# Optimization experiments

Measured on AMD Instinct MI355X. Metric: run time of the kernel, lower is better.

## Reference

```python
import jax, jax.numpy as jnp
import numpy as np

B, T, D = 2, 2048, 2048
H, KVH, HD = 32, 8, 64
N_REP = H // KVH


def setup_inputs() -> dict:
    key = jax.random.key(0)
    ks = jax.random.split(key, 7)
    x = jax.random.normal(ks[0], (B, T, D), dtype=jnp.float32)
    # rope tables: [max_seq, head_dim//2]
    cos = jax.random.uniform(ks[1], (T, HD // 2), dtype=jnp.float32, minval=-1.0, maxval=1.0)
    sin = jax.random.uniform(ks[2], (T, HD // 2), dtype=jnp.float32, minval=-1.0, maxval=1.0)
    s = 0.02
    wq = jax.random.normal(ks[3], (D, H * HD), dtype=jnp.float32) * s
    wk = jax.random.normal(ks[4], (D, KVH * HD), dtype=jnp.float32) * s
    wv = jax.random.normal(ks[5], (D, KVH * HD), dtype=jnp.float32) * s
    wo = jax.random.normal(ks[6], (H * HD, D), dtype=jnp.float32) * s
    return {"x": x, "cos": cos, "sin": sin, "wq": wq, "wk": wk, "wv": wv, "wo": wo}


def _rotate(t):
    h = t.shape[-1] // 2
    return jnp.concatenate([-t[..., h:], t[..., :h]], axis=-1)


def reference(x, cos, sin, wq, wk, wv, wo):
    b, t, _ = x.shape
    # projections -> [B, heads, T, HD]
    q = (x @ wq).reshape(b, t, H, HD).transpose(0, 2, 1, 3)
    k = (x @ wk).reshape(b, t, KVH, HD).transpose(0, 2, 1, 3)
    v = (x @ wv).reshape(b, t, KVH, HD).transpose(0, 2, 1, 3)
    # rope: cos/sin tiled (concat) to full head_dim, broadcast over batch/head
    cos_f = jnp.tile(cos[:t], (1, 2))[None, None]  # [1,1,T,HD]
    sin_f = jnp.tile(sin[:t], (1, 2))[None, None]
    q = q * cos_f + _rotate(q) * sin_f
    k = k * cos_f + _rotate(k) * sin_f
    # GQA: repeat kv heads
    k = jnp.repeat(k, N_REP, axis=1)
    v = jnp.repeat(v, N_REP, axis=1)
    scale = 1.0 / np.sqrt(HD).astype(np.float32)
    scores = jnp.einsum('bhqd,bhkd->bhqk', q, k) * scale
    causal = jnp.tril(jnp.ones((t, t), dtype=bool))
    scores = jnp.where(causal, scores, jnp.float32(-1e30))
    attn = jax.nn.softmax(scores, axis=-1)
    out = jnp.einsum('bhqk,bhkd->bhqd', attn, v)
    out = out.transpose(0, 2, 1, 3).reshape(b, t, H * HD)
    return out @ wo
```

## Files before the change

### kernel.cpp

```cpp
#include <hip/hip_runtime.h>
#include <hip/hip_bf16.h>
#include <cstdint>

typedef unsigned short u16;
typedef unsigned int u32;
typedef __bf16 bf16x8 __attribute__((ext_vector_type(8)));
typedef float f32x4 __attribute__((ext_vector_type(4)));

#define BATCH 2
#define SEQ 2048
#define DMODEL 2048
#define NH 32
#define NKVH 8
#define HD 64
#define NQROWS (BATCH*SEQ)
#define QCOLS (NH*HD)
#define KVCOLS (NKVH*HD)
#define NCAT (QCOLS+2*KVCOLS)

static __device__ __forceinline__ u16 f2bf(float f) {
  u32 u = __float_as_uint(f);
  return (u16)((u + 0x7fffu + ((u >> 16) & 1u)) >> 16);
}

#define GLOAD16(gp, lp) __builtin_amdgcn_global_load_lds( \
    (const __attribute__((address_space(1))) void*)(gp),  \
    (__attribute__((address_space(3))) void*)(lp), 16, 0, 0)

__global__ __launch_bounds__(256) void k_cvt_bf16(const float* __restrict__ in,
                                                  u16* __restrict__ out, int n4) {
  int i = blockIdx.x * 256 + threadIdx.x;
  if (i >= n4) return;
  float4 v = reinterpret_cast<const float4*>(in)[i];
  ushort4 o;
  o.x = f2bf(v.x); o.y = f2bf(v.y); o.z = f2bf(v.z); o.w = f2bf(v.w);
  reinterpret_cast<ushort4*>(out)[i] = o;
}

__global__ __launch_bounds__(256) void k_transpose_w(const float* __restrict__ in,
                                                     u16* __restrict__ out, int R, int C) {
  __shared__ float tile[32][33];
  int c0 = blockIdx.x * 32, r0 = blockIdx.y * 32;
  int tx = threadIdx.x, ty = threadIdx.y;
#pragma unroll
  for (int i = 0; i < 4; i++)
    tile[ty * 4 + i][tx] = in[(size_t)(r0 + ty * 4 + i) * C + c0 + tx];
  __syncthreads();
#pragma unroll
  for (int i = 0; i < 4; i++)
    out[(size_t)(c0 + ty * 4 + i) * R + r0 + tx] = f2bf(tile[tx][ty * 4 + i]);
}

template<int EPI>
__global__ __launch_bounds__(256) void k_gemm(const u16* __restrict__ A,
                                              const u16* __restrict__ BT,
                                              void* __restrict__ Cout,
                                              int M, int N, int K,
                                              const float* __restrict__ cosb,
                                              const float* __restrict__ sinb,
                                              u16* __restrict__ dstK,
                                              u16* __restrict__ dstV) {
  __shared__ __align__(16) u16 As[128 * 32];
  __shared__ __align__(16) u16 Bs[128 * 32];
  const int tid = threadIdx.x;
  const int w = tid >> 6, l = tid & 63;
  const int l15 = l & 15, l4 = l >> 4;
  const int m0 = blockIdx.y * 128, n0 = blockIdx.x * 128;
  const int wr = w >> 1, wc = w & 1;

  const u16* ga = A + (size_t)(m0 + w * 32 + (l >> 2)) * K + (l & 3) * 8;
  const u16* gb = BT + (size_t)(n0 + w * 32 + (l >> 2)) * K + (l & 3) * 8;
  u16* asb = &As[w * 1024];
  u16* bsb = &Bs[w * 1024];
  const int af_off = (wr * 64 + l15) * 32 + l4 * 8;
  const int bf_off = (wc * 64 + l15) * 32 + l4 * 8;

  f32x4 acc[4][4] = {};
  for (int kt = 0; kt < K; kt += 32) {
    GLOAD16(ga, asb);
    GLOAD16(ga + 16 * (size_t)K, asb + 512);
    GLOAD16(gb, bsb);
    GLOAD16(gb + 16 * (size_t)K, bsb + 512);
    ga += 32; gb += 32;
    __syncthreads();
    bf16x8 af[4], bfv[4];
#pragma unroll
    for (int mi = 0; mi < 4; mi++)
      af[mi] = *reinterpret_cast<const bf16x8*>(&As[af_off + mi * 512]);
#pragma unroll
    for (int ni = 0; ni < 4; ni++)
      bfv[ni] = *reinterpret_cast<const bf16x8*>(&Bs[bf_off + ni * 512]);
#pragma unroll
    for (int mi = 0; mi < 4; mi++)
#pragma unroll
      for (int ni = 0; ni < 4; ni++)
        acc[mi][ni] = __builtin_amdgcn_mfma_f32_16x16x32_bf16(af[mi], bfv[ni], acc[mi][ni], 0, 0, 0);
    __syncthreads();
  }

  const int row0 = m0 + wr * 64 + l4 * 4;
  const int col0 = n0 + wc * 64 + l15;
  if constexpr (EPI == 1) {
    float* C = (float*)Cout;
#pragma unroll
    for (int mi = 0; mi < 4; mi++)
#pragma unroll
      for (int ni = 0; ni < 4; ni++)
#pragma unroll
        for (int j = 0; j < 4; j++)
          C[(size_t)(row0 + mi * 16 + j) * N + col0 + ni * 16] = acc[mi][ni][j];
  } else {
    if (n0 < QCOLS + KVCOLS) {
#pragma unroll
      for (int mi = 0; mi < 4; mi++)
#pragma unroll
        for (int j = 0; j < 4; j++) {
          int t = (row0 + mi * 16 + j) & (SEQ - 1);
#pragma unroll
          for (int ni = 0; ni < 2; ni++) {
            int d = ni * 16 + l15;
            float c = cosb[t * 32 + d], s = sinb[t * 32 + d];
            float a = acc[mi][ni][j], bb = acc[mi][ni + 2][j];
            acc[mi][ni][j]     = a * c - bb * s;
            acc[mi][ni + 2][j] = bb * c + a * s;
          }
        }
      if (n0 < QCOLS) {
        u16* C = (u16*)Cout;
#pragma unroll
        for (int mi = 0; mi < 4; mi++)
#pragma unroll
          for (int ni = 0; ni < 4; ni++)
#pragma unroll
            for (int j = 0; j < 4; j++)
              C[(size_t)(row0 + mi * 16 + j) * QCOLS + col0 + ni * 16] = f2bf(acc[mi][ni][j]);
      } else {
        int kc0 = col0 - QCOLS;
#pragma unroll
        for (int mi = 0; mi < 4; mi++)
#pragma unroll
          for (int ni = 0; ni < 4; ni++)
#pragma unroll
            for (int j = 0; j < 4; j++)
              dstK[(size_t)(row0 + mi * 16 + j) * KVCOLS + kc0 + ni * 16] = f2bf(acc[mi][ni][j]);
      }
    } else {
      int vc0 = col0 - (QCOLS + KVCOLS);
#pragma unroll
      for (int mi = 0; mi < 4; mi++) {
        int row = row0 + mi * 16;
        int b = row >> 11, t = row & (SEQ - 1);
#pragma unroll
        for (int ni = 0; ni < 4; ni++) {
          ushort4 v;
          v.x = f2bf(acc[mi][ni][0]);
          v.y = f2bf(acc[mi][ni][1]);
          v.z = f2bf(acc[mi][ni][2]);
          v.w = f2bf(acc[mi][ni][3]);
          *reinterpret_cast<ushort4*>(&dstV[((size_t)b * KVCOLS + vc0 + ni * 16) * SEQ + t]) = v;
        }
      }
    }
  }
}

__global__ __launch_bounds__(256) void k_attn(const u16* __restrict__ Q,
                                              const u16* __restrict__ K,
                                              const u16* __restrict__ VT,
                                              u16* __restrict__ AO) {
  __shared__ __align__(16) u16 Ks[2][4096];
  __shared__ __align__(16) u16 Vs[2][4096];
  __shared__ __align__(16) u16 Plds[4][32][72];
  const int tid = threadIdx.x;
  const int w = tid >> 6, l = tid & 63;
  const int l15 = l & 15, l4 = l >> 4;
  const int bh = blockIdx.y;
  const int b = bh >> 5, h = bh & 31, g = h >> 2;
  const float cS = 0.125f * 1.44269504088896f;
  const int srow_w = w * 8 + (l >> 3);
  const int sslot = l & 7;

  const u16* Kbase = K + ((size_t)b * SEQ) * KVCOLS + g * 64;
  const u16* Vbase = VT + ((size_t)(b * KVCOLS + g * 64)) * SEQ;

  for (int half = 0; half < 2; half++) {
    const int qt = half ? (15 - blockIdx.x) : blockIdx.x;
    const int qrow0 = qt * 128 + w * 32;
    const int nkc = 2 * qt + 2;

    bf16x8 aQ[2][2];
#pragma unroll
    for (int mf = 0; mf < 2; mf++) {
      const u16* qp = Q + (size_t)(b * SEQ + qrow0 + mf * 16 + l15) * QCOLS + h * 64 + l4 * 8;
      aQ[mf][0] = *reinterpret_cast<const bf16x8*>(qp);
      aQ[mf][1] = *reinterpret_cast<const bf16x8*>(qp + 32);
    }
    f32x4 oacc[2][4] = {};
    float lsumP[2][4] = {};

#pragma unroll
    for (int i = 0; i < 2; i++) {
      int r = i * 32 + srow_w;
      int cs = sslot ^ (r & 7);
      GLOAD16(Kbase + (size_t)r * KVCOLS + cs * 8, &Ks[0][i * 2048 + w * 512 + l * 8]);
      GLOAD16(Vbase + (size_t)r * SEQ + cs * 8, &Vs[0][i * 2048 + w * 512 + l * 8]);
    }
    __syncthreads();

    for (int kc = 0; kc < nkc; kc++) {
      const int bi = kc & 1;
      if (kc + 1 < nkc) {
#pragma unroll
        for (int i = 0; i < 2; i++) {
          int r = i * 32 + srow_w;
          int cs = sslot ^ (r & 7);
          GLOAD16(Kbase + (size_t)((kc + 1) * 64 + r) * KVCOLS + cs * 8,
                  &Ks[bi ^ 1][i * 2048 + w * 512 + l * 8]);
          GLOAD16(Vbase + (size_t)r * SEQ + (kc + 1) * 64 + cs * 8,
                  &Vs[bi ^ 1][i * 2048 + w * 512 + l * 8]);
        }
      }
      const bool skip = (kc * 64 > qrow0 + 31);
      if (!skip) {
        f32x4 sacc[2][4] = {};
#pragma unroll
        for (int ni = 0; ni < 4; ni++) {
          int kr = ni * 16 + l15;
#pragma unroll
          for (int hh = 0; hh < 2; hh++) {
            int slot = (hh * 4 + l4) ^ (kr & 7);
            bf16x8 kf = *reinterpret_cast<const bf16x8*>(&Ks[bi][kr * 64 + slot * 8]);
            sacc[0][ni] = __builtin_amdgcn_mfma_f32_16x16x32_bf16(aQ[0][hh], kf, sacc[0][ni], 0, 0, 0);
            sacc[1][ni] = __builtin_amdgcn_mfma_f32_16x16x32_bf16(aQ[1][hh], kf, sacc[1][ni], 0, 0, 0);
          }
        }
        const bool diag = (kc * 64 + 63 > qrow0);
#pragma unroll
        for (int mf = 0; mf < 2; mf++) {
          int qr = qrow0 + mf * 16 + l4 * 4;
#pragma unroll
          for (int ni = 0; ni < 4; ni++) {
            int kcol = kc * 64 + ni * 16 + l15;
#pragma unroll
            for (int j = 0; j < 4; j++) {
              float pv = exp2f(sacc[mf][ni][j] * cS);
              if (diag && (kcol > qr + j)) pv = 0.f;
              lsumP[mf][j] += pv;
              __bf16 pb = (__bf16)pv;
              Plds[w][mf * 16 + l4 * 4 + j][ni * 16 + l15] = *(u16*)&pb;
            }
          }
        }
#pragma unroll
        for (int mf = 0; mf < 2; mf++) {
          bf16x8 pa0 = *reinterpret_cast<const bf16x8*>(&Plds[w][mf * 16 + l15][l4 * 8]);
          bf16x8 pa1 = *reinterpret_cast<const bf16x8*>(&Plds[w][mf * 16 + l15][32 + l4 * 8]);
#pragma unroll
          for (int no = 0; no < 4; no++) {
            int vr = no * 16 + l15;
            int s0 = l4 ^ (vr & 7);
            int s1 = (4 + l4) ^ (vr & 7);
            bf16x8 v0 = *reinterpret_cast<const bf16x8*>(&Vs[bi][vr * 64 + s0 * 8]);
            bf16x8 v1 = *reinterpret_cast<const bf16x8*>(&Vs[bi][vr * 64 + s1 * 8]);
            oacc[mf][no] = __builtin_amdgcn_mfma_f32_16x16x32_bf16(pa0, v0, oacc[mf][no], 0, 0, 0);
            oacc[mf][no] = __builtin_amdgcn_mfma_f32_16x16x32_bf16(pa1, v1, oacc[mf][no], 0, 0, 0);
          }
        }
      }
      __syncthreads();
    }
#pragma unroll
    for (int mf = 0; mf < 2; mf++) {
#pragma unroll
      for (int j = 0; j < 4; j++) {
        float v = lsumP[mf][j];
        v += __shfl_xor(v, 1, 16);
        v += __shfl_xor(v, 2, 16);
        v += __shfl_xor(v, 4, 16);
        v += __shfl_xor(v, 8, 16);
        float rv = 1.f / v;
        int row = b * SEQ + qrow0 + mf * 16 + l4 * 4 + j;
#pragma unroll
        for (int no = 0; no < 4; no++)
          AO[(size_t)row * QCOLS + h * 64 + no * 16 + l15] = f2bf(oacc[mf][no][j] * rv);
      }
    }
  }
}

extern "C" void kernel_launch(void* const* d_in, const int* in_sizes, int n_in,
                              void* d_out, int out_size, void* d_ws, size_t ws_size,
                              hipStream_t stream) {
  const float* x    = (const float*)d_in[0];
  const float* cosb = (const float*)d_in[1];
  const float* sinb = (const float*)d_in[2];
  const float* wq   = (const float*)d_in[3];
  const float* wk   = (const float*)d_in[4];
  const float* wv   = (const float*)d_in[5];
  const float* wo   = (const float*)d_in[6];
  float* out = (float*)d_out;

  char* ws = (char*)d_ws;
  size_t off = 0;
  auto alloc = [&](size_t bytes) -> void* {
    void* p = ws + off;
    off += (bytes + 255) & ~(size_t)255;
    return p;
  };
  u16* xb    = (u16*)alloc((size_t)NQROWS * DMODEL * 2);
  u16* wcatT = (u16*)alloc((size_t)NCAT * DMODEL * 2);
  u16* woT   = (u16*)alloc((size_t)DMODEL * QCOLS * 2);
  u16* Qb    = (u16*)alloc((size_t)NQROWS * QCOLS * 2);
  u16* Kb    = (u16*)alloc((size_t)NQROWS * KVCOLS * 2);
  u16* VTb   = (u16*)alloc((size_t)BATCH * KVCOLS * SEQ * 2);
  u16* AO    = (u16*)alloc((size_t)NQROWS * QCOLS * 2);

  k_cvt_bf16<<<dim3(NQROWS * DMODEL / 4 / 256), dim3(256), 0, stream>>>(x, xb, NQROWS * DMODEL / 4);
  k_transpose_w<<<dim3(QCOLS / 32, DMODEL / 32), dim3(32, 8), 0, stream>>>(wq, wcatT, DMODEL, QCOLS);
  k_transpose_w<<<dim3(KVCOLS / 32, DMODEL / 32), dim3(32, 8), 0, stream>>>(wk, wcatT + (size_t)QCOLS * DMODEL, DMODEL, KVCOLS);
  k_transpose_w<<<dim3(KVCOLS / 32, DMODEL / 32), dim3(32, 8), 0, stream>>>(wv, wcatT + (size_t)(QCOLS + KVCOLS) * DMODEL, DMODEL, KVCOLS);
  k_transpose_w<<<dim3(DMODEL / 32, QCOLS / 32), dim3(32, 8), 0, stream>>>(wo, woT, QCOLS, DMODEL);

  k_gemm<3><<<dim3(NCAT / 128, NQROWS / 128), 256, 0, stream>>>(
      xb, wcatT, Qb, NQROWS, NCAT, DMODEL, cosb, sinb, Kb, VTb);

  k_attn<<<dim3(8, BATCH * NH), 256, 0, stream>>>(Qb, Kb, VTb, AO);

  k_gemm<1><<<dim3(DMODEL / 128, NQROWS / 128), 256, 0, stream>>>(
      AO, woT, out, NQROWS, DMODEL, QCOLS, nullptr, nullptr, nullptr, nullptr);
}
```

Baseline: 249.3 us.

## Shrink attention query tile to 64 rows per block and double the grid

The attention kernel now gives each block 64 query rows (16 per wave) instead of 128 (32 per wave), and launches twice as many blocks. The paired tiles are folded as qt and 31-qt so per-block causal work stays balanced. Each block now walks fewer K/V chunks, and the per-wave skip check goes away because every chunk up to the diagonal is useful. This adds parallelism and occupancy, lowers register use, and cuts work wasted on masked chunks. In exchange, K/V tiles are reused across only half as many query rows, so K/V global traffic per query doubles.

```diff
diff --git a/kernel.cpp b/kernel.cpp
--- a/kernel.cpp
+++ b/kernel.cpp
@@ -170,7 +170,7 @@
                                               u16* __restrict__ AO) {
   __shared__ __align__(16) u16 Ks[2][4096];
   __shared__ __align__(16) u16 Vs[2][4096];
-  __shared__ __align__(16) u16 Plds[4][32][72];
+  __shared__ __align__(16) u16 Plds[4][16][72];
   const int tid = threadIdx.x;
   const int w = tid >> 6, l = tid & 63;
   const int l15 = l & 15, l4 = l >> 4;
@@ -184,19 +184,18 @@
   const u16* Vbase = VT + ((size_t)(b * KVCOLS + g * 64)) * SEQ;
 
   for (int half = 0; half < 2; half++) {
-    const int qt = half ? (15 - blockIdx.x) : blockIdx.x;
-    const int qrow0 = qt * 128 + w * 32;
-    const int nkc = 2 * qt + 2;
-
-    bf16x8 aQ[2][2];
-#pragma unroll
-    for (int mf = 0; mf < 2; mf++) {
-      const u16* qp = Q + (size_t)(b * SEQ + qrow0 + mf * 16 + l15) * QCOLS + h * 64 + l4 * 8;
-      aQ[mf][0] = *reinterpret_cast<const bf16x8*>(qp);
-      aQ[mf][1] = *reinterpret_cast<const bf16x8*>(qp + 32);
-    }
-    f32x4 oacc[2][4] = {};
-    float lsumP[2][4] = {};
+    const int qt = half ? (31 - blockIdx.x) : blockIdx.x;
+    const int qrow0 = qt * 64 + w * 16;
+    const int nkc = qt + 1;
+
+    bf16x8 aQ[2];
+    {
+      const u16* qp = Q + (size_t)(b * SEQ + qrow0 + l15) * QCOLS + h * 64 + l4 * 8;
+      aQ[0] = *reinterpret_cast<const bf16x8*>(qp);
+      aQ[1] = *reinterpret_cast<const bf16x8*>(qp + 32);
+    }
+    f32x4 oacc[4] = {};
+    float lsumP[4] = {};
 
 #pragma unroll
     for (int i = 0; i < 2; i++) {
@@ -220,70 +219,61 @@
                   &Vs[bi ^ 1][i * 2048 + w * 512 + l * 8]);
         }
       }
-      const bool skip = (kc * 64 > qrow0 + 31);
-      if (!skip) {
-        f32x4 sacc[2][4] = {};
+      f32x4 sacc[4] = {};
+#pragma unroll
+      for (int ni = 0; ni < 4; ni++) {
+        int kr = ni * 16 + l15;
+#pragma unroll
+        for (int hh = 0; hh < 2; hh++) {
+          int slot = (hh * 4 + l4) ^ (kr & 7);
+          bf16x8 kf = *reinterpret_cast<const bf16x8*>(&Ks[bi][kr * 64 + slot * 8]);
+          sacc[ni] = __builtin_amdgcn_mfma_f32_16x16x32_bf16(aQ[hh], kf, sacc[ni], 0, 0, 0);
+        }
+      }
+      const bool diag = (kc == qt);
+      {
+        int qr = qrow0 + l4 * 4;
 #pragma unroll
         for (int ni = 0; ni < 4; ni++) {
-          int kr = ni * 16 + l15;
-#pragma unroll
-          for (int hh = 0; hh < 2; hh++) {
-            int slot = (hh * 4 + l4) ^ (kr & 7);
-            bf16x8 kf = *reinterpret_cast<const bf16x8*>(&Ks[bi][kr * 64 + slot * 8]);
-            sacc[0][ni] = __builtin_amdgcn_mfma_f32_16x16x32_bf16(aQ[0][hh], kf, sacc[0][ni], 0, 0, 0);
-            sacc[1][ni] = __builtin_amdgcn_mfma_f32_16x16x32_bf16(aQ[1][hh], kf, sacc[1][ni], 0, 0, 0);
+          int kcol = kc * 64 + ni * 16 + l15;
+#pragma unroll
+          for (int j = 0; j < 4; j++) {
+            float pv = exp2f(sacc[ni][j] * cS);
+            if (diag && (kcol > qr + j)) pv = 0.f;
+            lsumP[j] += pv;
+            __bf16 pb = (__bf16)pv;
+            Plds[w][l4 * 4 + j][ni * 16 + l15] = *(u16*)&pb;
           }
         }
-        const bool diag = (kc * 64 + 63 > qrow0);
-#pragma unroll
-        for (int mf = 0; mf < 2; mf++) {
-          int qr = qrow0 + mf * 16 + l4 * 4;
-#pragma unroll
-          for (int ni = 0; ni < 4; ni++) {
-            int kcol = kc * 64 + ni * 16 + l15;
-#pragma unroll
-            for (int j = 0; j < 4; j++) {
-              float pv = exp2f(sacc[mf][ni][j] * cS);
-              if (diag && (kcol > qr + j)) pv = 0.f;
-              lsumP[mf][j] += pv;
-              __bf16 pb = (__bf16)pv;
-              Plds[w][mf * 16 + l4 * 4 + j][ni * 16 + l15] = *(u16*)&pb;
-            }
-          }
-        }
-#pragma unroll
-        for (int mf = 0; mf < 2; mf++) {
-          bf16x8 pa0 = *reinterpret_cast<const bf16x8*>(&Plds[w][mf * 16 + l15][l4 * 8]);
-          bf16x8 pa1 = *reinterpret_cast<const bf16x8*>(&Plds[w][mf * 16 + l15][32 + l4 * 8]);
-#pragma unroll
-          for (int no = 0; no < 4; no++) {
-            int vr = no * 16 + l15;
-            int s0 = l4 ^ (vr & 7);
-            int s1 = (4 + l4) ^ (vr & 7);
-            bf16x8 v0 = *reinterpret_cast<const bf16x8*>(&Vs[bi][vr * 64 + s0 * 8]);
-            bf16x8 v1 = *reinterpret_cast<const bf16x8*>(&Vs[bi][vr * 64 + s1 * 8]);
-            oacc[mf][no] = __builtin_amdgcn_mfma_f32_16x16x32_bf16(pa0, v0, oacc[mf][no], 0, 0, 0);
-            oacc[mf][no] = __builtin_amdgcn_mfma_f32_16x16x32_bf16(pa1, v1, oacc[mf][no], 0, 0, 0);
-          }
+      }
+      {
+        bf16x8 pa0 = *reinterpret_cast<const bf16x8*>(&Plds[w][l15][l4 * 8]);
+        bf16x8 pa1 = *reinterpret_cast<const bf16x8*>(&Plds[w][l15][32 + l4 * 8]);
+#pragma unroll
+        for (int no = 0; no < 4; no++) {
+          int vr = no * 16 + l15;
+          int s0 = l4 ^ (vr & 7);
+          int s1 = (4 + l4) ^ (vr & 7);
+          bf16x8 v0 = *reinterpret_cast<const bf16x8*>(&Vs[bi][vr * 64 + s0 * 8]);
+          bf16x8 v1 = *reinterpret_cast<const bf16x8*>(&Vs[bi][vr * 64 + s1 * 8]);
+          oacc[no] = __builtin_amdgcn_mfma_f32_16x16x32_bf16(pa0, v0, oacc[no], 0, 0, 0);
+          oacc[no] = __builtin_amdgcn_mfma_f32_16x16x32_bf16(pa1, v1, oacc[no], 0, 0, 0);
         }
       }
       __syncthreads();
     }
 #pragma unroll
-    for (int mf = 0; mf < 2; mf++) {
-#pragma unroll
-      for (int j = 0; j < 4; j++) {
-        float v = lsumP[mf][j];
-        v += __shfl_xor(v, 1, 16);
-        v += __shfl_xor(v, 2, 16);
-        v += __shfl_xor(v, 4, 16);
-        v += __shfl_xor(v, 8, 16);
-        float rv = 1.f / v;
-        int row = b * SEQ + qrow0 + mf * 16 + l4 * 4 + j;
-#pragma unroll
-        for (int no = 0; no < 4; no++)
-          AO[(size_t)row * QCOLS + h * 64 + no * 16 + l15] = f2bf(oacc[mf][no][j] * rv);
-      }
+    for (int j = 0; j < 4; j++) {
+      float v = lsumP[j];
+      v += __shfl_xor(v, 1, 16);
+      v += __shfl_xor(v, 2, 16);
+      v += __shfl_xor(v, 4, 16);
+      v += __shfl_xor(v, 8, 16);
+      float rv = 1.f / v;
+      int row = b * SEQ + qrow0 + l4 * 4 + j;
+#pragma unroll
+      for (int no = 0; no < 4; no++)
+        AO[(size_t)row * QCOLS + h * 64 + no * 16 + l15] = f2bf(oacc[no][j] * rv);
     }
   }
 }
@@ -324,7 +314,7 @@
   k_gemm<3><<<dim3(NCAT / 128, NQROWS / 128), 256, 0, stream>>>(
       xb, wcatT, Qb, NQROWS, NCAT, DMODEL, cosb, sinb, Kb, VTb);
 
-  k_attn<<<dim3(8, BATCH * NH), 256, 0, stream>>>(Qb, Kb, VTb, AO);
+  k_attn<<<dim3(16, BATCH * NH), 256, 0, stream>>>(Qb, Kb, VTb, AO);
 
   k_gemm<1><<<dim3(DMODEL / 128, NQROWS / 128), 256, 0, stream>>>(
       AO, woT, out, NQROWS, DMODEL, QCOLS, nullptr, nullptr, nullptr, nullptr);
```

New measurement: 245.8 us. Within noise of the previous version (-1.4%).
